# Optimization experiments

Measured on AMD Instinct MI355X. Metric: run time of the kernel, lower is better.

The kernel has to match this reference:

```python
import jax, jax.numpy as jnp
import numpy as np

D_MODEL = 2048
NUM_HEADS = 16
HEAD_DIM = D_MODEL // NUM_HEADS
B, T = 4, 2048


def setup_inputs() -> dict:
    key = jax.random.key(0)
    ks = jax.random.split(key, 9)
    s = 1.0 / np.sqrt(D_MODEL)
    inp = {"x": jax.random.normal(ks[0], (B, T, D_MODEL), dtype=jnp.float32)}
    for i, name in enumerate(["q", "k", "v", "o"]):
        inp[f"W{name}"] = jax.random.uniform(ks[1 + 2 * i], (D_MODEL, D_MODEL), minval=-s, maxval=s, dtype=jnp.float32)
        inp[f"b{name}"] = jax.random.uniform(ks[2 + 2 * i], (D_MODEL,), minval=-s, maxval=s, dtype=jnp.float32)
    return inp


def reference(x, Wq, bq, Wk, bk, Wv, bv, Wo, bo):
    Bx, Tx, _ = x.shape
    H, Dh = NUM_HEADS, HEAD_DIM
    # torch Linear: y = x @ W.T + b
    q = (x @ Wq.T + bq).reshape(Bx, Tx, H, Dh).transpose(0, 2, 1, 3)  # [B,H,T,D]
    k = (x @ Wk.T + bk).reshape(Bx, Tx, H, Dh).transpose(0, 2, 1, 3)
    v = (x @ Wv.T + bv).reshape(Bx, Tx, H, Dh).transpose(0, 2, 1, 3)
    scale = 1.0 / np.sqrt(Dh).astype(np.float32)
    scores = jnp.einsum('bhqd,bhkd->bhqk', q, k) * scale  # [B,H,T,T] (no causal mask, as in source)
    attn = jax.nn.softmax(scores, axis=-1)
    out = jnp.einsum('bhqk,bhkd->bhqd', attn, v)  # [B,H,T,D]
    out = out.transpose(0, 2, 1, 3).reshape(Bx, Tx, H * Dh)
    return out @ Wo.T + bo
```

## Files before the change

kernel.cpp:

```cpp
#include <hip/hip_runtime.h>
#include <hip/hip_bf16.h>

typedef __bf16 bf16x8 __attribute__((ext_vector_type(8)));
typedef __bf16 bf16x4 __attribute__((ext_vector_type(4)));
typedef float floatx4 __attribute__((ext_vector_type(4)));

#define MFMA16(a, b, c) __builtin_amdgcn_mfma_f32_16x16x32_bf16((a), (b), (c), 0, 0, 0)

#define GLOAD16(g, l) __builtin_amdgcn_global_load_lds( \
    (const __attribute__((address_space(1))) unsigned int*)(g), \
    (__attribute__((address_space(3))) unsigned int*)(l), 16, 0, 0)

static constexpr int DM = 2048, NH = 16, HD = 128, BATCH = 4, SEQ = 2048;
static constexpr int MROWS = BATCH * SEQ;
static constexpr float SCALE = 0.08838834764831845f;
static constexpr float PMAX = 3.0f;

static constexpr size_t XE = (size_t)MROWS * DM;
static constexpr size_t WE = (size_t)DM * DM;

__global__ __launch_bounds__(256) void cvt_all(
    const float* __restrict__ x, const float* __restrict__ Wq,
    const float* __restrict__ Wk, const float* __restrict__ Wv,
    const float* __restrict__ Wo, __bf16* __restrict__ dst) {
  const size_t total = XE + 4 * WE;
  size_t stride = (size_t)gridDim.x * 256 * 8;
  for (size_t i = ((size_t)blockIdx.x * 256 + threadIdx.x) * 8; i < total; i += stride) {
    const float* src;
    size_t off;
    if (i < XE) { src = x; off = i; }
    else {
      size_t j = i - XE;
      int seg = (int)(j / WE);
      off = j - (size_t)seg * WE;
      src = seg == 0 ? Wq : (seg == 1 ? Wk : (seg == 2 ? Wv : Wo));
    }
    float4 a = *reinterpret_cast<const float4*>(src + off);
    float4 b = *reinterpret_cast<const float4*>(src + off + 4);
    bf16x8 r;
    r[0] = (__bf16)a.x; r[1] = (__bf16)a.y; r[2] = (__bf16)a.z; r[3] = (__bf16)a.w;
    r[4] = (__bf16)b.x; r[5] = (__bf16)b.y; r[6] = (__bf16)b.z; r[7] = (__bf16)b.w;
    *reinterpret_cast<bf16x8*>(dst + i) = r;
  }
}

__device__ __forceinline__ void gemm128_core(
    const __bf16* __restrict__ A, const __bf16* __restrict__ W,
    unsigned short* sA, unsigned short* sW,
    int tm, int tn, floatx4 (&acc)[4][4]) {
  const int tid = threadIdx.x;
  const int wave = tid >> 6, lane = tid & 63;
  const int q = lane >> 4, ml = lane & 15;
  const int waveM = (wave >> 1) * 64, waveN = (wave & 1) * 64;
  const int lrow = lane >> 3, cdst = lane & 7;
  const int csrc = cdst ^ (lrow & 7);

  for (int k0 = 0; k0 < DM; k0 += 64) {
    __syncthreads();
#pragma unroll
    for (int i = 0; i < 4; ++i) {
      int r0 = wave * 32 + i * 8;
      GLOAD16(A + (size_t)(tm + r0 + lrow) * DM + k0 + csrc * 8, &sA[r0 * 64]);
      GLOAD16(W + (size_t)(tn + r0 + lrow) * DM + k0 + csrc * 8, &sW[r0 * 64]);
    }
    __syncthreads();
#pragma unroll
    for (int s = 0; s < 2; ++s) {
      bf16x8 aF[4], bF[4];
#pragma unroll
      for (int t = 0; t < 4; ++t)
        aF[t] = *reinterpret_cast<const bf16x8*>(
            &sA[(waveM + t * 16 + ml) * 64 + (((s * 4 + q) ^ (ml & 7)) * 8)]);
#pragma unroll
      for (int t = 0; t < 4; ++t)
        bF[t] = *reinterpret_cast<const bf16x8*>(
            &sW[(waveN + t * 16 + ml) * 64 + (((s * 4 + q) ^ (ml & 7)) * 8)]);
#pragma unroll
      for (int rt = 0; rt < 4; ++rt)
#pragma unroll
        for (int ct = 0; ct < 4; ++ct)
          acc[rt][ct] = MFMA16(aF[rt], bF[ct], acc[rt][ct]);
    }
  }
}

__global__ __launch_bounds__(256) void qkv_gemm(
    const __bf16* __restrict__ X,
    const __bf16* __restrict__ Wq, const __bf16* __restrict__ Wk,
    const __bf16* __restrict__ Wv,
    const float* __restrict__ bq, const float* __restrict__ bk,
    const float* __restrict__ bv,
    __bf16* __restrict__ qh, __bf16* __restrict__ kh, __bf16* __restrict__ vt) {
  __shared__ unsigned short sA[128 * 64];
  __shared__ unsigned short sW[128 * 64];
  const int which = blockIdx.x >> 4;
  const int tn = (blockIdx.x & 15) * 128;
  const int tm = blockIdx.y * 128;
  const __bf16* W = which == 0 ? Wq : (which == 1 ? Wk : Wv);
  const float* bias = which == 0 ? bq : (which == 1 ? bk : bv);

  floatx4 acc[4][4] = {};
  gemm128_core(X, W, sA, sW, tm, tn, acc);

  const int tid = threadIdx.x, wave = tid >> 6, lane = tid & 63;
  const int q = lane >> 4, ml = lane & 15;
  const int waveM = (wave >> 1) * 64, waveN = (wave & 1) * 64;
#pragma unroll
  for (int ct = 0; ct < 4; ++ct) {
    int n = tn + waveN + ct * 16 + ml;
    float bv_ = bias[n];
    int h = n >> 7, d = n & 127;
#pragma unroll
    for (int rt = 0; rt < 4; ++rt) {
      int m0 = tm + waveM + rt * 16 + q * 4;
      int b = m0 >> 11, t = m0 & 2047;
      if (which < 2) {
        __bf16* dst = which == 0 ? qh : kh;
#pragma unroll
        for (int r = 0; r < 4; ++r)
          dst[((size_t)(b * 16 + h) * SEQ + t + r) * HD + d] = (__bf16)(acc[rt][ct][r] + bv_);
      } else {
        bf16x4 pk;
#pragma unroll
        for (int r = 0; r < 4; ++r) pk[r] = (__bf16)(acc[rt][ct][r] + bv_);
        *reinterpret_cast<bf16x4*>(vt + (size_t)((b * 16 + h) * 128 + d) * SEQ + t) = pk;
      }
    }
  }
}

__global__ __launch_bounds__(256) void proj_gemm(
    const __bf16* __restrict__ A, const __bf16* __restrict__ W,
    const float* __restrict__ bias, float* __restrict__ out) {
  __shared__ unsigned short sA[128 * 64];
  __shared__ unsigned short sW[128 * 64];
  const int tn = blockIdx.x * 128;
  const int tm = blockIdx.y * 128;

  floatx4 acc[4][4] = {};
  gemm128_core(A, W, sA, sW, tm, tn, acc);

  const int tid = threadIdx.x, wave = tid >> 6, lane = tid & 63;
  const int q = lane >> 4, ml = lane & 15;
  const int waveM = (wave >> 1) * 64, waveN = (wave & 1) * 64;
#pragma unroll
  for (int ct = 0; ct < 4; ++ct) {
    int n = tn + waveN + ct * 16 + ml;
    float bv_ = bias[n];
#pragma unroll
    for (int rt = 0; rt < 4; ++rt) {
      int m0 = tm + waveM + rt * 16 + q * 4;
#pragma unroll
      for (int r = 0; r < 4; ++r)
        out[(size_t)(m0 + r) * DM + n] = acc[rt][ct][r] + bv_;
    }
  }
}

__global__ __launch_bounds__(512) void mha_attn(
    const __bf16* __restrict__ Q, const __bf16* __restrict__ Kg,
    const __bf16* __restrict__ Vt, __bf16* __restrict__ O) {
  __shared__ unsigned short sK[64 * 128];
  __shared__ unsigned short sV[128 * 64];
  __shared__ unsigned short sP[128 * 72];

  const int tid = threadIdx.x;
  const int bh = blockIdx.x;
  const int t0 = blockIdx.y * 128;
  const int wave = tid >> 6, lane = tid & 63;
  const int q = lane >> 4, ml = lane & 15;
  const int wrow = wave * 16;

  bf16x8 qf[4];
  {
    const __bf16* qrow = Q + ((size_t)bh * SEQ + t0 + wrow + ml) * HD;
#pragma unroll
    for (int s = 0; s < 4; ++s)
      qf[s] = *reinterpret_cast<const bf16x8*>(qrow + s * 32 + q * 8);
  }

  floatx4 oacc[8] = {};
  float lsum[4] = {0.f, 0.f, 0.f, 0.f};

  const __bf16* kbase = Kg + (size_t)bh * SEQ * HD;
  const __bf16* vbase = Vt + (size_t)bh * HD * SEQ;
  const int lrow4 = lane >> 4, c16 = lane & 15;
  const int lrow8 = lane >> 3, c8 = lane & 7;

  for (int kt = 0; kt < SEQ / 64; ++kt) {
    const int key0 = kt * 64;
    __syncthreads();
#pragma unroll
    for (int i = 0; i < 2; ++i) {
      int kr0 = wave * 8 + i * 4;
      int kc = c16 ^ ((i * 4 + lrow4) & 7);
      GLOAD16(kbase + (size_t)(key0 + kr0 + lrow4) * HD + kc * 8, &sK[kr0 * 128]);
      int vr0 = wave * 16 + i * 8;
      int vc = c8 ^ (lrow8 & 7);
      GLOAD16(vbase + (size_t)(vr0 + lrow8) * SEQ + key0 + vc * 8, &sV[vr0 * 64]);
    }
    __syncthreads();

    floatx4 sacc[4] = {};
#pragma unroll
    for (int s = 0; s < 4; ++s) {
#pragma unroll
      for (int ct = 0; ct < 4; ++ct) {
        bf16x8 kf = *reinterpret_cast<const bf16x8*>(
            &sK[(ct * 16 + ml) * 128 + (((s * 4 + q) ^ (ml & 7)) * 8)]);
        sacc[ct] = MFMA16(qf[s], kf, sacc[ct]);
      }
    }

#pragma unroll
    for (int ct = 0; ct < 4; ++ct) {
#pragma unroll
      for (int r = 0; r < 4; ++r) {
        float p = __expf(fmaf(sacc[ct][r], SCALE, -PMAX));
        sacc[ct][r] = p;
        lsum[r] += p;
        __bf16 pb = (__bf16)p;
        sP[(wrow + q * 4 + r) * 72 + ct * 16 + ml] = __builtin_bit_cast(unsigned short, pb);
      }
    }

#pragma unroll
    for (int s = 0; s < 2; ++s) {
      bf16x8 pf = *reinterpret_cast<const bf16x8*>(&sP[(wrow + ml) * 72 + s * 32 + q * 8]);
#pragma unroll
      for (int ot = 0; ot < 8; ++ot) {
        bf16x8 vf = *reinterpret_cast<const bf16x8*>(
            &sV[(ot * 16 + ml) * 64 + (((s * 4 + q) ^ (ml & 7)) * 8)]);
        oacc[ot] = MFMA16(pf, vf, oacc[ot]);
      }
    }
  }

#pragma unroll
  for (int r = 0; r < 4; ++r) {
    float s = lsum[r];
    s += __shfl_xor(s, 1); s += __shfl_xor(s, 2);
    s += __shfl_xor(s, 4); s += __shfl_xor(s, 8);
    lsum[r] = 1.0f / s;
  }
  const int b = bh >> 4, h = bh & 15;
  __bf16* obase = O + ((size_t)b * SEQ + t0 + wrow) * DM + h * HD;
#pragma unroll
  for (int ot = 0; ot < 8; ++ot) {
    int d = ot * 16 + ml;
#pragma unroll
    for (int r = 0; r < 4; ++r)
      obase[(size_t)(q * 4 + r) * DM + d] = (__bf16)(oacc[ot][r] * lsum[r]);
  }
}

__device__ inline bf16x8 ld8s(const float* p) {
  float4 a = *reinterpret_cast<const float4*>(p);
  float4 b = *reinterpret_cast<const float4*>(p + 4);
  bf16x8 r;
  r[0] = (__bf16)a.x; r[1] = (__bf16)a.y; r[2] = (__bf16)a.z; r[3] = (__bf16)a.w;
  r[4] = (__bf16)b.x; r[5] = (__bf16)b.y; r[6] = (__bf16)b.z; r[7] = (__bf16)b.w;
  return r;
}
__device__ inline bf16x8 ld8s(const __bf16* p) {
  int4 v = *reinterpret_cast<const int4*>(p);
  return __builtin_bit_cast(bf16x8, v);
}

template <typename TA>
__global__ __launch_bounds__(256) void gemm_slow(
    const TA* __restrict__ A, const float* __restrict__ W,
    const float* __restrict__ bias, void* __restrict__ C, int mode, int out_f32) {
  __shared__ unsigned short sA[128 * 72];
  __shared__ unsigned short sW[128 * 72];
  const int tid = threadIdx.x;
  const int tn = blockIdx.x * 128, tm = blockIdx.y * 128;
  const int wave = tid >> 6, lane = tid & 63;
  const int q = lane >> 4, ml = lane & 15;
  const int waveM = (wave >> 1) * 64, waveN = (wave & 1) * 64;
  const int srow = tid >> 3, sc8 = tid & 7;
  floatx4 acc[4][4] = {};
  for (int k0 = 0; k0 < DM; k0 += 64) {
    bf16x8 va[4], vb[4];
#pragma unroll
    for (int i = 0; i < 4; ++i) {
      int row = srow + 32 * i;
      va[i] = ld8s(A + (size_t)(tm + row) * DM + k0 + sc8 * 8);
      vb[i] = ld8s(W + (size_t)(tn + row) * DM + k0 + sc8 * 8);
    }
    __syncthreads();
#pragma unroll
    for (int i = 0; i < 4; ++i) {
      int row = srow + 32 * i;
      *reinterpret_cast<int4*>(&sA[row * 72 + sc8 * 8]) = __builtin_bit_cast(int4, va[i]);
      *reinterpret_cast<int4*>(&sW[row * 72 + sc8 * 8]) = __builtin_bit_cast(int4, vb[i]);
    }
    __syncthreads();
#pragma unroll
    for (int s = 0; s < 2; ++s) {
      bf16x8 aF[4], bF[4];
#pragma unroll
      for (int t = 0; t < 4; ++t)
        aF[t] = *reinterpret_cast<const bf16x8*>(&sA[(waveM + t * 16 + ml) * 72 + s * 32 + q * 8]);
#pragma unroll
      for (int t = 0; t < 4; ++t)
        bF[t] = *reinterpret_cast<const bf16x8*>(&sW[(waveN + t * 16 + ml) * 72 + s * 32 + q * 8]);
#pragma unroll
      for (int rt = 0; rt < 4; ++rt)
#pragma unroll
        for (int ct = 0; ct < 4; ++ct)
          acc[rt][ct] = MFMA16(aF[rt], bF[ct], acc[rt][ct]);
    }
  }
#pragma unroll
  for (int ct = 0; ct < 4; ++ct) {
    int n = tn + waveN + ct * 16 + ml;
    float bv = bias[n];
    int h = n >> 7, d = n & 127;
#pragma unroll
    for (int rt = 0; rt < 4; ++rt) {
      int m0 = tm + waveM + rt * 16 + q * 4;
      int b = m0 >> 11, t = m0 & 2047;
      if (mode == 0) {
        if (out_f32) {
#pragma unroll
          for (int r = 0; r < 4; ++r)
            ((float*)C)[(size_t)(m0 + r) * DM + n] = acc[rt][ct][r] + bv;
        } else {
#pragma unroll
          for (int r = 0; r < 4; ++r)
            ((__bf16*)C)[(size_t)(m0 + r) * DM + n] = (__bf16)(acc[rt][ct][r] + bv);
        }
      } else if (mode == 1) {
        bf16x4 pk;
#pragma unroll
        for (int r = 0; r < 4; ++r) pk[r] = (__bf16)(acc[rt][ct][r] + bv);
        *reinterpret_cast<bf16x4*>((__bf16*)C + (size_t)((b * 16 + h) * 128 + d) * SEQ + t) = pk;
      } else {
#pragma unroll
        for (int r = 0; r < 4; ++r)
          ((__bf16*)C)[((size_t)(b * 16 + h) * SEQ + t + r) * HD + d] =
              (__bf16)(acc[rt][ct][r] + bv);
      }
    }
  }
}

extern "C" void kernel_launch(void* const* d_in, const int* in_sizes, int n_in,
                              void* d_out, int out_size, void* d_ws, size_t ws_size,
                              hipStream_t stream) {
  const float* x  = (const float*)d_in[0];
  const float* Wq = (const float*)d_in[1]; const float* bq = (const float*)d_in[2];
  const float* Wk = (const float*)d_in[3]; const float* bk = (const float*)d_in[4];
  const float* Wv = (const float*)d_in[5]; const float* bv = (const float*)d_in[6];
  const float* Wo = (const float*)d_in[7]; const float* bo = (const float*)d_in[8];

  const size_t needA = 64 + 2 * (4 * XE + 4 * WE);
  dim3 gq(48, 64), gp(16, 64), ga(BATCH * NH, SEQ / 128);

  if (ws_size >= needA + 256) {
    __bf16* xc  = (__bf16*)((char*)d_ws + 64);
    __bf16* Wqc = xc + XE;
    __bf16* Wkc = Wqc + WE;
    __bf16* Wvc = Wkc + WE;
    __bf16* Woc = Wvc + WE;
    __bf16* qh  = Woc + WE;
    __bf16* kh  = qh + XE;
    __bf16* vt  = kh + XE;
    __bf16* aw  = xc;

    cvt_all<<<4096, 256, 0, stream>>>(x, Wq, Wk, Wv, Wo, xc);
    qkv_gemm<<<gq, 256, 0, stream>>>(xc, Wqc, Wkc, Wvc, bq, bk, bv, qh, kh, vt);
    mha_attn<<<ga, 512, 0, stream>>>(qh, kh, vt, aw);
    proj_gemm<<<gp, 256, 0, stream>>>(aw, Woc, bo, (float*)d_out);
  } else {
    __bf16* qh = (__bf16*)((char*)d_ws + 64);
    __bf16* kh = qh + XE;
    __bf16* vt = kh + XE;
    __bf16* aw = vt + XE;
    gemm_slow<float><<<gp, 256, 0, stream>>>(x, Wq, bq, qh, 2, 0);
    gemm_slow<float><<<gp, 256, 0, stream>>>(x, Wk, bk, kh, 2, 0);
    gemm_slow<float><<<gp, 256, 0, stream>>>(x, Wv, bv, vt, 1, 0);
    mha_attn<<<ga, 512, 0, stream>>>(qh, kh, vt, aw);
    gemm_slow<__bf16><<<gp, 256, 0, stream>>>(aw, Wo, bo, d_out, 0, 1);
  }
}
```

Measured before the change: 727.2 us.

## Load weight and K/V fragments straight from global, enlarge GEMM M-tile to 256

The GEMM core now uses a 256-row A tile staged in LDS, while each wave loads its W fragments directly from global into registers, so the weight LDS buffer is gone. The attention kernel drops LDS staging of K and V: each wave reads K and V fragments from global memory and handles two 16-row query tiles, running with 256 threads and a two-blocks-per-CU hint. This aims to remove LDS traffic and barriers and to reuse each fragment across more MFMAs. In exchange it relies on L2/L1 caching for the redundant global K/V/W reads and raises register pressure.

```diff
diff --git a/kernel.cpp b/kernel.cpp
--- a/kernel.cpp
+++ b/kernel.cpp
@@ -44,74 +44,76 @@
   }
 }
 
-__device__ __forceinline__ void gemm128_core(
+__device__ __forceinline__ void gemm256_core(
     const __bf16* __restrict__ A, const __bf16* __restrict__ W,
-    unsigned short* sA, unsigned short* sW,
-    int tm, int tn, floatx4 (&acc)[4][4]) {
+    unsigned short* sA, int tm, int tn, floatx4 (&acc)[8][4]) {
   const int tid = threadIdx.x;
   const int wave = tid >> 6, lane = tid & 63;
   const int q = lane >> 4, ml = lane & 15;
-  const int waveM = (wave >> 1) * 64, waveN = (wave & 1) * 64;
+  const int waveM = (wave >> 1) * 128, waveN = (wave & 1) * 64;
   const int lrow = lane >> 3, cdst = lane & 7;
-  const int csrc = cdst ^ (lrow & 7);
+  const int csrc = cdst ^ lrow;
+
+  const __bf16* wbase = W + (size_t)(tn + waveN + ml) * DM + q * 8;
 
   for (int k0 = 0; k0 < DM; k0 += 64) {
     __syncthreads();
-#pragma unroll
-    for (int i = 0; i < 4; ++i) {
-      int r0 = wave * 32 + i * 8;
+    bf16x8 bF[2][4];
+#pragma unroll
+    for (int s = 0; s < 2; ++s)
+#pragma unroll
+      for (int ct = 0; ct < 4; ++ct)
+        bF[s][ct] = *reinterpret_cast<const bf16x8*>(
+            wbase + (size_t)ct * 16 * DM + k0 + s * 32);
+#pragma unroll
+    for (int i = 0; i < 8; ++i) {
+      int r0 = i * 32 + wave * 8;
       GLOAD16(A + (size_t)(tm + r0 + lrow) * DM + k0 + csrc * 8, &sA[r0 * 64]);
-      GLOAD16(W + (size_t)(tn + r0 + lrow) * DM + k0 + csrc * 8, &sW[r0 * 64]);
     }
     __syncthreads();
 #pragma unroll
     for (int s = 0; s < 2; ++s) {
-      bf16x8 aF[4], bF[4];
-#pragma unroll
-      for (int t = 0; t < 4; ++t)
+      bf16x8 aF[8];
+#pragma unroll
+      for (int t = 0; t < 8; ++t)
         aF[t] = *reinterpret_cast<const bf16x8*>(
             &sA[(waveM + t * 16 + ml) * 64 + (((s * 4 + q) ^ (ml & 7)) * 8)]);
 #pragma unroll
-      for (int t = 0; t < 4; ++t)
-        bF[t] = *reinterpret_cast<const bf16x8*>(
-            &sW[(waveN + t * 16 + ml) * 64 + (((s * 4 + q) ^ (ml & 7)) * 8)]);
-#pragma unroll
-      for (int rt = 0; rt < 4; ++rt)
+      for (int rt = 0; rt < 8; ++rt)
 #pragma unroll
         for (int ct = 0; ct < 4; ++ct)
-          acc[rt][ct] = MFMA16(aF[rt], bF[ct], acc[rt][ct]);
-    }
-  }
-}
-
-__global__ __launch_bounds__(256) void qkv_gemm(
+          acc[rt][ct] = MFMA16(aF[rt], bF[s][ct], acc[rt][ct]);
+    }
+  }
+}
+
+__global__ __launch_bounds__(256, 2) void qkv_gemm(
     const __bf16* __restrict__ X,
     const __bf16* __restrict__ Wq, const __bf16* __restrict__ Wk,
     const __bf16* __restrict__ Wv,
     const float* __restrict__ bq, const float* __restrict__ bk,
     const float* __restrict__ bv,
     __bf16* __restrict__ qh, __bf16* __restrict__ kh, __bf16* __restrict__ vt) {
-  __shared__ unsigned short sA[128 * 64];
-  __shared__ unsigned short sW[128 * 64];
+  __shared__ unsigned short sA[256 * 64];
   const int which = blockIdx.x >> 4;
   const int tn = (blockIdx.x & 15) * 128;
-  const int tm = blockIdx.y * 128;
+  const int tm = blockIdx.y * 256;
   const __bf16* W = which == 0 ? Wq : (which == 1 ? Wk : Wv);
   const float* bias = which == 0 ? bq : (which == 1 ? bk : bv);
 
-  floatx4 acc[4][4] = {};
-  gemm128_core(X, W, sA, sW, tm, tn, acc);
+  floatx4 acc[8][4] = {};
+  gemm256_core(X, W, sA, tm, tn, acc);
 
   const int tid = threadIdx.x, wave = tid >> 6, lane = tid & 63;
   const int q = lane >> 4, ml = lane & 15;
-  const int waveM = (wave >> 1) * 64, waveN = (wave & 1) * 64;
+  const int waveM = (wave >> 1) * 128, waveN = (wave & 1) * 64;
 #pragma unroll
   for (int ct = 0; ct < 4; ++ct) {
     int n = tn + waveN + ct * 16 + ml;
     float bv_ = bias[n];
     int h = n >> 7, d = n & 127;
 #pragma unroll
-    for (int rt = 0; rt < 4; ++rt) {
+    for (int rt = 0; rt < 8; ++rt) {
       int m0 = tm + waveM + rt * 16 + q * 4;
       int b = m0 >> 11, t = m0 & 2047;
       if (which < 2) {
@@ -129,26 +131,25 @@
   }
 }
 
-__global__ __launch_bounds__(256) void proj_gemm(
+__global__ __launch_bounds__(256, 2) void proj_gemm(
     const __bf16* __restrict__ A, const __bf16* __restrict__ W,
     const float* __restrict__ bias, float* __restrict__ out) {
-  __shared__ unsigned short sA[128 * 64];
-  __shared__ unsigned short sW[128 * 64];
+  __shared__ unsigned short sA[256 * 64];
   const int tn = blockIdx.x * 128;
-  const int tm = blockIdx.y * 128;
-
-  floatx4 acc[4][4] = {};
-  gemm128_core(A, W, sA, sW, tm, tn, acc);
+  const int tm = blockIdx.y * 256;
+
+  floatx4 acc[8][4] = {};
+  gemm256_core(A, W, sA, tm, tn, acc);
 
   const int tid = threadIdx.x, wave = tid >> 6, lane = tid & 63;
   const int q = lane >> 4, ml = lane & 15;
-  const int waveM = (wave >> 1) * 64, waveN = (wave & 1) * 64;
+  const int waveM = (wave >> 1) * 128, waveN = (wave & 1) * 64;
 #pragma unroll
   for (int ct = 0; ct < 4; ++ct) {
     int n = tn + waveN + ct * 16 + ml;
     float bv_ = bias[n];
 #pragma unroll
-    for (int rt = 0; rt < 4; ++rt) {
+    for (int rt = 0; rt < 8; ++rt) {
       int m0 = tm + waveM + rt * 16 + q * 4;
 #pragma unroll
       for (int r = 0; r < 4; ++r)
@@ -157,11 +158,9 @@
   }
 }
 
-__global__ __launch_bounds__(512) void mha_attn(
+__global__ __launch_bounds__(256, 2) void mha_attn(
     const __bf16* __restrict__ Q, const __bf16* __restrict__ Kg,
     const __bf16* __restrict__ Vt, __bf16* __restrict__ O) {
-  __shared__ unsigned short sK[64 * 128];
-  __shared__ unsigned short sV[128 * 64];
   __shared__ unsigned short sP[128 * 72];
 
   const int tid = threadIdx.x;
@@ -169,88 +168,92 @@
   const int t0 = blockIdx.y * 128;
   const int wave = tid >> 6, lane = tid & 63;
   const int q = lane >> 4, ml = lane & 15;
-  const int wrow = wave * 16;
-
-  bf16x8 qf[4];
+  const int wrow = wave * 32;
+
+  bf16x8 qf[2][4];
   {
-    const __bf16* qrow = Q + ((size_t)bh * SEQ + t0 + wrow + ml) * HD;
-#pragma unroll
-    for (int s = 0; s < 4; ++s)
-      qf[s] = *reinterpret_cast<const bf16x8*>(qrow + s * 32 + q * 8);
-  }
-
-  floatx4 oacc[8] = {};
-  float lsum[4] = {0.f, 0.f, 0.f, 0.f};
-
-  const __bf16* kbase = Kg + (size_t)bh * SEQ * HD;
-  const __bf16* vbase = Vt + (size_t)bh * HD * SEQ;
-  const int lrow4 = lane >> 4, c16 = lane & 15;
-  const int lrow8 = lane >> 3, c8 = lane & 7;
+    const __bf16* qbase = Q + ((size_t)bh * SEQ + t0 + wrow) * HD;
+#pragma unroll
+    for (int qt = 0; qt < 2; ++qt)
+#pragma unroll
+      for (int s = 0; s < 4; ++s)
+        qf[qt][s] = *reinterpret_cast<const bf16x8*>(
+            qbase + (size_t)(qt * 16 + ml) * HD + s * 32 + q * 8);
+  }
+
+  floatx4 oacc[2][8] = {};
+  float lsum[2][4] = {};
+
+  const __bf16* kbase = Kg + (size_t)bh * SEQ * HD + q * 8;
+  const __bf16* vbase = Vt + (size_t)bh * HD * SEQ + q * 8;
 
   for (int kt = 0; kt < SEQ / 64; ++kt) {
     const int key0 = kt * 64;
-    __syncthreads();
-#pragma unroll
-    for (int i = 0; i < 2; ++i) {
-      int kr0 = wave * 8 + i * 4;
-      int kc = c16 ^ ((i * 4 + lrow4) & 7);
-      GLOAD16(kbase + (size_t)(key0 + kr0 + lrow4) * HD + kc * 8, &sK[kr0 * 128]);
-      int vr0 = wave * 16 + i * 8;
-      int vc = c8 ^ (lrow8 & 7);
-      GLOAD16(vbase + (size_t)(vr0 + lrow8) * SEQ + key0 + vc * 8, &sV[vr0 * 64]);
-    }
-    __syncthreads();
-
-    floatx4 sacc[4] = {};
+
+    floatx4 sacc[2][4] = {};
 #pragma unroll
     for (int s = 0; s < 4; ++s) {
-#pragma unroll
-      for (int ct = 0; ct < 4; ++ct) {
-        bf16x8 kf = *reinterpret_cast<const bf16x8*>(
-            &sK[(ct * 16 + ml) * 128 + (((s * 4 + q) ^ (ml & 7)) * 8)]);
-        sacc[ct] = MFMA16(qf[s], kf, sacc[ct]);
-      }
-    }
-
-#pragma unroll
-    for (int ct = 0; ct < 4; ++ct) {
-#pragma unroll
-      for (int r = 0; r < 4; ++r) {
-        float p = __expf(fmaf(sacc[ct][r], SCALE, -PMAX));
-        sacc[ct][r] = p;
-        lsum[r] += p;
-        __bf16 pb = (__bf16)p;
-        sP[(wrow + q * 4 + r) * 72 + ct * 16 + ml] = __builtin_bit_cast(unsigned short, pb);
-      }
-    }
+      bf16x8 kf[4];
+#pragma unroll
+      for (int ct = 0; ct < 4; ++ct)
+        kf[ct] = *reinterpret_cast<const bf16x8*>(
+            kbase + (size_t)(key0 + ct * 16 + ml) * HD + s * 32);
+#pragma unroll
+      for (int qt = 0; qt < 2; ++qt)
+#pragma unroll
+        for (int ct = 0; ct < 4; ++ct)
+          sacc[qt][ct] = MFMA16(qf[qt][s], kf[ct], sacc[qt][ct]);
+    }
+
+#pragma unroll
+    for (int qt = 0; qt < 2; ++qt)
+#pragma unroll
+      for (int ct = 0; ct < 4; ++ct)
+#pragma unroll
+        for (int r = 0; r < 4; ++r) {
+          float p = __expf(fmaf(sacc[qt][ct][r], SCALE, -PMAX));
+          lsum[qt][r] += p;
+          __bf16 pb = (__bf16)p;
+          sP[(wrow + qt * 16 + q * 4 + r) * 72 + ct * 16 + ml] =
+              __builtin_bit_cast(unsigned short, pb);
+        }
 
 #pragma unroll
     for (int s = 0; s < 2; ++s) {
-      bf16x8 pf = *reinterpret_cast<const bf16x8*>(&sP[(wrow + ml) * 72 + s * 32 + q * 8]);
+      bf16x8 pf[2];
+#pragma unroll
+      for (int qt = 0; qt < 2; ++qt)
+        pf[qt] = *reinterpret_cast<const bf16x8*>(
+            &sP[(wrow + qt * 16 + ml) * 72 + s * 32 + q * 8]);
 #pragma unroll
       for (int ot = 0; ot < 8; ++ot) {
         bf16x8 vf = *reinterpret_cast<const bf16x8*>(
-            &sV[(ot * 16 + ml) * 64 + (((s * 4 + q) ^ (ml & 7)) * 8)]);
-        oacc[ot] = MFMA16(pf, vf, oacc[ot]);
+            vbase + (size_t)(ot * 16 + ml) * SEQ + key0 + s * 32);
+#pragma unroll
+        for (int qt = 0; qt < 2; ++qt)
+          oacc[qt][ot] = MFMA16(pf[qt], vf, oacc[qt][ot]);
       }
     }
   }
 
-#pragma unroll
-  for (int r = 0; r < 4; ++r) {
-    float s = lsum[r];
-    s += __shfl_xor(s, 1); s += __shfl_xor(s, 2);
-    s += __shfl_xor(s, 4); s += __shfl_xor(s, 8);
-    lsum[r] = 1.0f / s;
-  }
   const int b = bh >> 4, h = bh & 15;
-  __bf16* obase = O + ((size_t)b * SEQ + t0 + wrow) * DM + h * HD;
-#pragma unroll
-  for (int ot = 0; ot < 8; ++ot) {
-    int d = ot * 16 + ml;
-#pragma unroll
-    for (int r = 0; r < 4; ++r)
-      obase[(size_t)(q * 4 + r) * DM + d] = (__bf16)(oacc[ot][r] * lsum[r]);
+#pragma unroll
+  for (int qt = 0; qt < 2; ++qt) {
+#pragma unroll
+    for (int r = 0; r < 4; ++r) {
+      float s = lsum[qt][r];
+      s += __shfl_xor(s, 1); s += __shfl_xor(s, 2);
+      s += __shfl_xor(s, 4); s += __shfl_xor(s, 8);
+      lsum[qt][r] = 1.0f / s;
+    }
+    __bf16* obase = O + ((size_t)b * SEQ + t0 + wrow + qt * 16) * DM + h * HD;
+#pragma unroll
+    for (int ot = 0; ot < 8; ++ot) {
+      int d = ot * 16 + ml;
+#pragma unroll
+      for (int r = 0; r < 4; ++r)
+        obase[(size_t)(q * 4 + r) * DM + d] = (__bf16)(oacc[qt][ot][r] * lsum[qt][r]);
+    }
   }
 }
 
@@ -356,7 +359,7 @@
   const float* Wo = (const float*)d_in[7]; const float* bo = (const float*)d_in[8];
 
   const size_t needA = 64 + 2 * (4 * XE + 4 * WE);
-  dim3 gq(48, 64), gp(16, 64), ga(BATCH * NH, SEQ / 128);
+  dim3 gq(48, 32), gp(16, 32), ga(BATCH * NH, SEQ / 128);
 
   if (ws_size >= needA + 256) {
     __bf16* xc  = (__bf16*)((char*)d_ws + 64);
@@ -371,17 +374,18 @@
 
     cvt_all<<<4096, 256, 0, stream>>>(x, Wq, Wk, Wv, Wo, xc);
     qkv_gemm<<<gq, 256, 0, stream>>>(xc, Wqc, Wkc, Wvc, bq, bk, bv, qh, kh, vt);
-    mha_attn<<<ga, 512, 0, stream>>>(qh, kh, vt, aw);
+    mha_attn<<<ga, 256, 0, stream>>>(qh, kh, vt, aw);
     proj_gemm<<<gp, 256, 0, stream>>>(aw, Woc, bo, (float*)d_out);
   } else {
+    dim3 gs(16, 64);
     __bf16* qh = (__bf16*)((char*)d_ws + 64);
     __bf16* kh = qh + XE;
     __bf16* vt = kh + XE;
     __bf16* aw = vt + XE;
-    gemm_slow<float><<<gp, 256, 0, stream>>>(x, Wq, bq, qh, 2, 0);
-    gemm_slow<float><<<gp, 256, 0, stream>>>(x, Wk, bk, kh, 2, 0);
-    gemm_slow<float><<<gp, 256, 0, stream>>>(x, Wv, bv, vt, 1, 0);
-    mha_attn<<<ga, 512, 0, stream>>>(qh, kh, vt, aw);
-    gemm_slow<__bf16><<<gp, 256, 0, stream>>>(aw, Wo, bo, d_out, 0, 1);
-  }
-}
+    gemm_slow<float><<<gs, 256, 0, stream>>>(x, Wq, bq, qh, 2, 0);
+    gemm_slow<float><<<gs, 256, 0, stream>>>(x, Wk, bk, kh, 2, 0);
+    gemm_slow<float><<<gs, 256, 0, stream>>>(x, Wv, bv, vt, 1, 0);
+    mha_attn<<<ga, 256, 0, stream>>>(qh, kh, vt, aw);
+    gemm_slow<__bf16><<<gs, 256, 0, stream>>>(aw, Wo, bo, d_out, 0, 1);
+  }
+}
```

Measured after the change: 1.083 ms. 49.0% more time.
